# Optimization experiments

Hardware: AMD Instinct MI355X
Metric: run time of the kernel (lower is better)

## Reference

```python
import jax, jax.numpy as jnp
from jax import lax
import numpy as np

K_TOP = 100
NMS_THRESH = 0.5
SUBJECT_CATEGORY_ID = 0


def box_cxcywh_to_xyxy(b):
    cx, cy, w, h = b[..., 0], b[..., 1], b[..., 2], b[..., 3]
    return jnp.stack([cx - 0.5 * w, cy - 0.5 * h, cx + 0.5 * w, cy + 0.5 * h], axis=-1)


def _pairwise_iou(boxes):
    # boxes: [K,4] xyxy; uses the +1 pixel convention from the original numpy NMS
    x1, y1, x2, y2 = boxes[:, 0], boxes[:, 1], boxes[:, 2], boxes[:, 3]
    area = (x2 - x1 + 1.0) * (y2 - y1 + 1.0)
    xx1 = jnp.maximum(x1[:, None], x1[None, :])
    yy1 = jnp.maximum(y1[:, None], y1[None, :])
    xx2 = jnp.minimum(x2[:, None], x2[None, :])
    yy2 = jnp.minimum(y2[:, None], y2[None, :])
    w = jnp.maximum(0.0, xx2 - xx1 + 1.0)
    h = jnp.maximum(0.0, yy2 - yy1 + 1.0)
    inter = w * h
    union = area[:, None] + area[None, :] - inter
    return inter / union


def _nms_keep(sub_boxes, obj_boxes, obj_labels, hoi_scores):
    # Greedy grouped pairwise NMS for one image.
    # Grouping key degenerates to object label (subject cat and verb-row are constant).
    K = sub_boxes.shape[0]
    max_scores = hoi_scores.max(axis=-1)
    order = jnp.argsort(-max_scores)
    ovr = _pairwise_iou(sub_boxes) * _pairwise_iou(obj_boxes)  # [K,K]
    same_group = obj_labels[:, None] == obj_labels[None, :]
    ovr = jnp.where(same_group, ovr, 0.0)
    ovr_s = ovr[order][:, order]
    upper = jnp.triu(jnp.ones((K, K), dtype=bool), k=1)
    sup_mat = (ovr_s > NMS_THRESH) & upper  # suppression only of later (lower-score) items

    def body(i, st):
        suppressed, keep = st
        ki = jnp.logical_not(suppressed[i])
        keep = keep.at[i].set(ki)
        suppressed = suppressed | (ki & sup_mat[i])
        return suppressed, keep

    _, keep_sorted = lax.fori_loop(0, K, body, (jnp.zeros(K, bool), jnp.zeros(K, bool)))
    return jnp.zeros(K, bool).at[order].set(keep_sorted)


def setup_inputs() -> dict:
    key = jax.random.key(0)
    k1, k2, k3, k4, k5, k6 = jax.random.split(key, 6)
    B, Q, C, V = 256, 300, 81, 117
    return {
        "pred_obj_logits": jax.random.normal(k1, (B, Q, C), dtype=jnp.float32),
        "pred_verb_logits": jax.random.normal(k2, (B, Q, V), dtype=jnp.float32),
        "pred_sub_boxes": jax.random.uniform(k3, (B, Q, 4), dtype=jnp.float32),
        "pred_obj_boxes": jax.random.uniform(k4, (B, Q, 4), dtype=jnp.float32),
        "correct_mat": (jax.random.uniform(k5, (V, C), dtype=jnp.float32) > 0.3).astype(jnp.float32),
        "target_sizes": jax.random.randint(k6, (B, 2), 200, 640, dtype=jnp.int32),
    }


def reference(pred_obj_logits, pred_verb_logits, pred_sub_boxes, pred_obj_boxes, correct_mat, target_sizes):
    B, Q, C = pred_obj_logits.shape
    V = pred_verb_logits.shape[-1]

    obj_prob = jax.nn.softmax(pred_obj_logits, axis=-1)       # [B,Q,C]  (no_obj=False)
    verb_scores = jax.nn.sigmoid(pred_verb_logits)            # [B,Q,V]

    topk_values, topk_indexes = lax.top_k(obj_prob.reshape(B, Q * C), K_TOP)  # [B,100]
    topk_boxes = topk_indexes // C
    obj_labels = topk_indexes % C

    vs = jnp.take_along_axis(verb_scores, topk_boxes[..., None], axis=1)      # [B,100,V]
    ob = jnp.take_along_axis(pred_obj_boxes, topk_boxes[..., None], axis=1)   # [B,100,4]
    sb = jnp.take_along_axis(pred_sub_boxes, topk_boxes[..., None], axis=1)

    img_h = target_sizes[:, 0].astype(jnp.float32)
    img_w = target_sizes[:, 1].astype(jnp.float32)
    scale_fct = jnp.stack([img_w, img_h, img_w, img_h], axis=1)  # [B,4]
    sub_boxes = box_cxcywh_to_xyxy(sb) * scale_fct[:, None, :]
    obj_boxes = box_cxcywh_to_xyxy(ob) * scale_fct[:, None, :]

    hoi_scores = vs * topk_values[..., None]                    # [B,100,V]
    # masks[b,k,v] = correct_mat[v, obj_labels[b,k]]
    masks = correct_mat.T[obj_labels]                           # [B,100,V]
    hoi_scores = hoi_scores * masks

    keep = jax.vmap(_nms_keep)(sub_boxes, obj_boxes, obj_labels, hoi_scores)  # [B,100] bool
    final_scores = hoi_scores * keep[..., None].astype(hoi_scores.dtype)

    return final_scores, topk_values, obj_labels, sub_boxes, obj_boxes, keep
```

## Files before the change

kernel.cpp:

```cpp
#include <hip/hip_runtime.h>
#include <cmath>

#pragma clang fp contract(off)

#define NT 1024
constexpr int B_ = 256, Q_ = 300, C_ = 81, V_ = 117, K_ = 100;
constexpr int QC_ = Q_ * C_;
constexpr int KV_ = K_ * V_;
constexpr int CAP = 1024;

using u32 = unsigned int;
using u64 = unsigned long long;
using u16 = unsigned short;
using u8  = unsigned char;

constexpr u32 PCUT_BITS = 0x3C000000u;
constexpr int BIN0 = 480;
constexpr int NB   = 64;

constexpr int OFF_HS   = 0;
constexpr int OFF_HIST = 48600;
constexpr int OFF_RMAX = OFF_HIST + 8192;
constexpr int OFF_RINV = OFF_RMAX + 1200;
constexpr int OFF_BSUB = OFF_RINV + 1208;
constexpr int OFF_BOBJ = OFF_BSUB + 1600;
constexpr int OFF_SUPR = OFF_BOBJ + 1600;
constexpr int OFF_SELV = OFF_SUPR + 1600;
constexpr int OFF_SELI = OFF_SELV + 400;
constexpr int OFF_MAXB = OFF_SELI + 400;
constexpr int OFF_ORD  = OFF_MAXB + 400;
constexpr int OFF_LAB  = OFF_ORD + 104;
constexpr int OFF_MISC = OFF_LAB + 104;
constexpr int SMEM_SZ  = OFF_MISC + 48;
static_assert(SMEM_SZ <= 65536, "LDS overflow");
static_assert((OFF_BSUB & 15) == 0 && (OFF_BOBJ & 15) == 0, "b128 align");

__device__ __forceinline__ u64 shfl_xor_u64(u64 v, int mask) {
    u32 lo = (u32)v, hi = (u32)(v >> 32);
    lo = (u32)__shfl_xor((int)lo, mask, 64);
    hi = (u32)__shfl_xor((int)hi, mask, 64);
    return ((u64)hi << 32) | lo;
}

template <int CTRL>
__device__ __forceinline__ int dpp_i(int x) {
    return __builtin_amdgcn_update_dpp(0, x, CTRL, 0xF, 0xF, true);
}
__device__ __forceinline__ float bfly16(float x){ return __int_as_float(__builtin_amdgcn_ds_swizzle(__float_as_int(x), 0x401F)); }
__device__ __forceinline__ float bfly8 (float x){ return __int_as_float(dpp_i<0x128>(__float_as_int(x))); }
__device__ __forceinline__ float bfly4 (float x){ return __int_as_float(__builtin_amdgcn_ds_swizzle(__float_as_int(x), 0x101F)); }
__device__ __forceinline__ float bfly2 (float x){ return __int_as_float(dpp_i<0x4E>(__float_as_int(x))); }
__device__ __forceinline__ float bfly1 (float x){ return __int_as_float(dpp_i<0xB1>(__float_as_int(x))); }
__device__ __forceinline__ int ibfly4(int x){ return __builtin_amdgcn_ds_swizzle(x, 0x101F); }
__device__ __forceinline__ int ibfly2(int x){ return dpp_i<0x4E>(x); }
__device__ __forceinline__ int ibfly1(int x){ return dpp_i<0xB1>(x); }

__device__ __forceinline__ float iou4(float4 a, float4 b, float areaSum) {
    float xx1 = fmaxf(a.x, b.x);
    float yy1 = fmaxf(a.y, b.y);
    float xx2 = fminf(a.z, b.z);
    float yy2 = fminf(a.w, b.w);
    float w = fmaxf(0.f, xx2 - xx1 + 1.f);
    float h = fmaxf(0.f, yy2 - yy1 + 1.f);
    float inter = w * h;
    return inter / (areaSum - inter);
}

__global__ __launch_bounds__(NT, 4) void hoi_kernel(
    const float* __restrict__ obj_logits,
    const float* __restrict__ verb_logits,
    const float* __restrict__ sub_boxes_in,
    const float* __restrict__ obj_boxes_in,
    const float* __restrict__ cm,
    const int*   __restrict__ tsizes,
    float* __restrict__ out)
{
    const int b = blockIdx.x;
    const int tid = threadIdx.x;

    __shared__ __align__(16) u8 smem[SMEM_SZ];
    float* hs      = (float*)(smem + OFF_HS);
    u32*   hist    = (u32*)(smem + OFF_HIST);
    u64*   cand    = (u64*)(smem + OFF_HIST);
    float* asub    = (float*)(smem + OFF_HIST);
    float* aobj    = (float*)(smem + OFF_HIST + 512);
    float* rowmax  = (float*)(smem + OFF_RMAX);
    float* rinv    = (float*)(smem + OFF_RINV);
    float (*bsub)[4]   = (float(*)[4])(smem + OFF_BSUB);
    float (*bobj)[4]   = (float(*)[4])(smem + OFF_BOBJ);
    u32   (*supcol)[4] = (u32(*)[4])(smem + OFF_SUPR);
    float* sel_val = (float*)(smem + OFF_SELV);
    u32*   sel_idx = (u32*)(smem + OFF_SELI);
    u32*   maxbits = (u32*)(smem + OFF_MAXB);
    u8*    order8  = (u8*)(smem + OFF_ORD);
    u8*    lab8    = (u8*)(smem + OFF_LAB);
    u32*   skeep     = (u32*)(smem + OFF_MISC);
    u32*   keep_bits = (u32*)(smem + OFF_MISC + 16);
    u32*   s_cnt     = (u32*)(smem + OFF_MISC + 32);
    int*   sT        = (int*)(smem + OFF_MISC + 36);
    u64*   wred    = (u64*)(smem + OFF_BOBJ);
    u64*   s_prev  = (u64*)(smem + OFF_SUPR);

    const float* lg = obj_logits + (size_t)b * QC_;

    if (tid < NB) hist[tid] = 0;
    if (tid == 0) *s_cnt = 0;
    __syncthreads();

    const int g = tid >> 5, l = tid & 31;
    const bool have2 = (l < C_ - 64);
    u32 cmask = 0;
    {
        float v0[10], v1[10], v2[10];
        #pragma unroll
        for (int s = 0; s < 10; ++s) {
            int r = g + 32 * s;
            const float* row = lg + (size_t)((r < Q_ ? r : Q_ - 1) * C_);
            v0[s] = row[l];
            v1[s] = row[l + 32];
            v2[s] = have2 ? row[l + 64] : -INFINITY;
        }
        float m[10];
        #pragma unroll
        for (int s = 0; s < 10; ++s) m[s] = fmaxf(fmaxf(v0[s], v1[s]), v2[s]);
        #pragma unroll
        for (int s = 0; s < 10; ++s) m[s] = fmaxf(m[s], bfly16(m[s]));
        #pragma unroll
        for (int s = 0; s < 10; ++s) m[s] = fmaxf(m[s], bfly8(m[s]));
        #pragma unroll
        for (int s = 0; s < 10; ++s) m[s] = fmaxf(m[s], bfly4(m[s]));
        #pragma unroll
        for (int s = 0; s < 10; ++s) m[s] = fmaxf(m[s], bfly2(m[s]));
        #pragma unroll
        for (int s = 0; s < 10; ++s) m[s] = fmaxf(m[s], bfly1(m[s]));
        float e0[10], e1[10], e2[10], sm[10];
        #pragma unroll
        for (int s = 0; s < 10; ++s) {
            e0[s] = expf(v0[s] - m[s]);
            e1[s] = expf(v1[s] - m[s]);
            e2[s] = have2 ? expf(v2[s] - m[s]) : 0.f;
            sm[s] = e0[s] + e1[s] + e2[s];
        }
        #pragma unroll
        for (int s = 0; s < 10; ++s) sm[s] += bfly16(sm[s]);
        #pragma unroll
        for (int s = 0; s < 10; ++s) sm[s] += bfly8(sm[s]);
        #pragma unroll
        for (int s = 0; s < 10; ++s) sm[s] += bfly4(sm[s]);
        #pragma unroll
        for (int s = 0; s < 10; ++s) sm[s] += bfly2(sm[s]);
        #pragma unroll
        for (int s = 0; s < 10; ++s) sm[s] += bfly1(sm[s]);
        #pragma unroll
        for (int s = 0; s < 10; ++s) {
            int r = g + 32 * s;
            if (r < Q_) {
                float ri = 1.f / sm[s];
                float p0 = e0[s] * ri, p1 = e1[s] * ri;
                u32 x0 = __float_as_uint(p0), x1 = __float_as_uint(p1);
                if (x0 >= PCUT_BITS) {
                    atomicAdd(&hist[(x0 >> 21) - BIN0], 1u);
                    cmask |= 1u << (3 * s);
                }
                if (x1 >= PCUT_BITS) {
                    atomicAdd(&hist[(x1 >> 21) - BIN0], 1u);
                    cmask |= 1u << (3 * s + 1);
                }
                if (have2) {
                    float p2 = e2[s] * ri;
                    u32 x2 = __float_as_uint(p2);
                    if (x2 >= PCUT_BITS) {
                        atomicAdd(&hist[(x2 >> 21) - BIN0], 1u);
                        cmask |= 1u << (3 * s + 2);
                    }
                }
                if (l == 0) { rowmax[r] = m[s]; rinv[r] = ri; }
            }
        }
    }
    __syncthreads();

    if (tid < 64) {
        u32 suf = hist[tid];
        #pragma unroll
        for (int off = 1; off < 64; off <<= 1) {
            u32 o = (u32)__shfl_down((int)suf, off, 64);
            suf += (tid + off < 64) ? o : 0;
        }
        u32 nxt = (u32)__shfl_down((int)suf, 1, 64);
        if (tid == 63) nxt = 0;
        if (suf >= (u32)K_ && nxt < (u32)K_) *sT = BIN0 + tid;
    }
    __syncthreads();
    const int T = *sT;

    u32 mk = cmask;
    while (mk) {
        int bpos = (int)__builtin_ctz(mk);
        mk &= mk - 1;
        int s = (bpos * 171) >> 9;
        int c = bpos - 3 * s;
        int r = g + 32 * s;
        int col = l + 32 * c;
        int i = r * C_ + col;
        float p = expf(lg[i] - rowmax[r]) * rinv[r];
        u32 xb = __float_as_uint(p);
        if ((int)(xb >> 21) >= T) {
            u32 pos = atomicAdd(s_cnt, 1u);
            if (pos < (u32)CAP)
                cand[pos] = ((u64)xb << 32) | (u32)(~i);
        }
    }
    __syncthreads();
    const int ncand = (int)*s_cnt;

    auto cswap = [](u64& a, u64& bb, bool up) {
        if ((a > bb) == up) { u64 t = a; a = bb; bb = t; }
    };

    if (ncand <= 256) {
        if (tid < 64) {
            u64 v0 = (tid < ncand) ? cand[tid] : 0ull;
            u64 v1 = (64 + tid < ncand) ? cand[64 + tid] : 0ull;
            u64 v2 = (128 + tid < ncand) ? cand[128 + tid] : 0ull;
            u64 v3 = (192 + tid < ncand) ? cand[192 + tid] : 0ull;
            for (int k = 2; k <= 256; k <<= 1) {
                for (int j = k >> 1; j > 0; j >>= 1) {
                    if (j == 128) {
                        cswap(v0, v2, true);
                        cswap(v1, v3, true);
                    } else if (j == 64) {
                        cswap(v0, v1, true);
                        cswap(v2, v3, (k == 256));
                    } else {
                        auto step = [&](u64& v, int ebase) {
                            u64 pv = shfl_xor_u64(v, j);
                            int e = ebase + tid;
                            bool up = ((e & k) == 0);
                            bool lower = ((e & j) == 0);
                            u64 mn = v < pv ? v : pv;
                            u64 mx = v < pv ? pv : v;
                            v = (lower == up) ? mn : mx;
                        };
                        step(v0, 0); step(v1, 64); step(v2, 128); step(v3, 192);
                    }
                }
            }
            int e2 = 128 + tid;
            if (e2 >= 156) {
                int t = 255 - e2;
                sel_val[t] = __uint_as_float((u32)(v2 >> 32));
                sel_idx[t] = ~(u32)v2;
            }
            int t3 = 255 - (192 + tid);
            sel_val[t3] = __uint_as_float((u32)(v3 >> 32));
            sel_idx[t3] = ~(u32)v3;
        }
    } else if (ncand <= CAP) {
        for (int e = tid; e < CAP; e += NT)
            if (e >= ncand) cand[e] = 0;
        __syncthreads();
        for (int k = 2; k <= CAP; k <<= 1) {
            for (int j = k >> 1; j > 0; j >>= 1) {
                int e = tid, partner = e ^ j;
                if (partner > e) {
                    u64 a = cand[e], bb = cand[partner];
                    bool up = ((e & k) == 0);
                    if ((a > bb) == up) { cand[e] = bb; cand[partner] = a; }
                }
                __syncthreads();
            }
        }
        if (tid < K_) {
            u64 m = cand[CAP - 1 - tid];
            sel_val[tid] = __uint_as_float((u32)(m >> 32));
            sel_idx[tid] = ~(u32)m;
        }
    } else {
        if (tid == 0) *s_prev = ~0ull;
        __syncthreads();
        for (int r = 0; r < K_; r++) {
            u64 prev = *s_prev;
            u64 local = 0;
            for (int i = tid; i < QC_; i += NT) {
                int q = i / C_;
                float p = expf(lg[i] - rowmax[q]) * rinv[q];
                u64 key = ((u64)__float_as_uint(p) << 32) | (u32)(~i);
                if (key < prev && key > local) local = key;
            }
            for (int off = 32; off > 0; off >>= 1) {
                u64 o = shfl_xor_u64(local, off);
                if (o > local) local = o;
            }
            if ((tid & 63) == 0) wred[tid >> 6] = local;
            __syncthreads();
            if (tid == 0) {
                u64 m = wred[0];
                for (int wv = 1; wv < 16; wv++) if (wred[wv] > m) m = wred[wv];
                *s_prev = m;
                u32 idx = ~(u32)m;
                if (idx >= (u32)QC_) idx = 0;
                sel_val[r] = __uint_as_float((u32)(m >> 32));
                sel_idx[r] = idx;
            }
            __syncthreads();
        }
    }
    __syncthreads();

    if (tid < 800) {
        int c = tid >> 3, j = tid & 7;
        u32 idx = sel_idx[c];
        int q = (int)idx / C_, lab = (int)idx - q * C_;
        const float* vrow = verb_logits + ((size_t)b * Q_ + q) * V_;
        float sv = sel_val[c];
        float xv[15], cv[15];
        #pragma unroll
        for (int k = 0; k < 15; ++k) {
            int v = j + 8 * k;
            int vc = v < V_ ? v : V_ - 1;
            xv[k] = vrow[vc];
            cv[k] = cm[vc * C_ + lab];
        }
        float m = 0.f;
        #pragma unroll
        for (int k = 0; k < 15; ++k) {
            int v = j + 8 * k;
            if (v < V_) {
                float hv = (1.f / (1.f + expf(-xv[k]))) * sv * cv[k];
                hs[c * V_ + v] = hv;
                m = fmaxf(m, hv);
            }
        }
        m = fmaxf(m, bfly4(m));
        m = fmaxf(m, bfly2(m));
        m = fmaxf(m, bfly1(m));
        if (j == 0) { maxbits[c] = __float_as_uint(m); lab8[c] = (u8)lab; }
    } else if (tid < 900) {
        int t = tid - 800;
        int idx = (int)sel_idx[t];
        int q = idx / C_;
        float iw = (float)tsizes[b * 2 + 1];
        float ih = (float)tsizes[b * 2 + 0];
        float4 sb = ((const float4*)sub_boxes_in)[(size_t)b * Q_ + q];
        float x1 = (sb.x - 0.5f * sb.z) * iw, y1 = (sb.y - 0.5f * sb.w) * ih;
        float x2 = (sb.x + 0.5f * sb.z) * iw, y2 = (sb.y + 0.5f * sb.w) * ih;
        bsub[t][0] = x1; bsub[t][1] = y1; bsub[t][2] = x2; bsub[t][3] = y2;
        asub[t] = (x2 - x1 + 1.f) * (y2 - y1 + 1.f);
        supcol[t][0] = 0; supcol[t][1] = 0; supcol[t][2] = 0; supcol[t][3] = 0;
    } else if (tid < 1000) {
        int t = tid - 900;
        int idx = (int)sel_idx[t];
        int q = idx / C_;
        float iw = (float)tsizes[b * 2 + 1];
        float ih = (float)tsizes[b * 2 + 0];
        float4 ob = ((const float4*)obj_boxes_in)[(size_t)b * Q_ + q];
        float x1 = (ob.x - 0.5f * ob.z) * iw, y1 = (ob.y - 0.5f * ob.w) * ih;
        float x2 = (ob.x + 0.5f * ob.z) * iw, y2 = (ob.y + 0.5f * ob.w) * ih;
        bobj[t][0] = x1; bobj[t][1] = y1; bobj[t][2] = x2; bobj[t][3] = y2;
        aobj[t] = (x2 - x1 + 1.f) * (y2 - y1 + 1.f);
    } else if (tid < 1004) {
        keep_bits[tid - 1000] = 0;
    }
    __syncthreads();

    if (tid < 800) {
        int r = tid >> 3, j = tid & 7;
        u64 kr = ((u64)maxbits[r] << 32) | (u32)(~r);
        int rank = 0;
        for (int k = 0; k < 13; k++) {
            int jj = j * 13 + k;
            if (jj < K_) {
                u64 kj = ((u64)maxbits[jj] << 32) | (u32)(~jj);
                rank += (kj > kr) ? 1 : 0;
            }
        }
        rank += ibfly4(rank);
        rank += ibfly2(rank);
        rank += ibfly1(rank);
        if (j == 0) order8[rank] = (u8)r;
    }
    __syncthreads();

    float* o0 = out;
    float* o1 = out + (size_t)B_ * KV_;
    float* o2 = o1 + (size_t)B_ * K_;
    float* o3 = o2 + (size_t)B_ * K_;
    float* o4 = o3 + (size_t)B_ * K_ * 4;
    float* o5 = o4 + (size_t)B_ * K_ * 4;

    if (tid < K_) {
        o1[(size_t)b * K_ + tid] = sel_val[tid];
        o2[(size_t)b * K_ + tid] = (float)(sel_idx[tid] % (u32)C_);
    }
    if (tid >= 128 && tid < 128 + K_ * 4) {
        int t = tid - 128;
        int r = t >> 2, k = t & 3;
        o3[((size_t)b * K_) * 4 + t] = bsub[r][k];
        o4[((size_t)b * K_) * 4 + t] = bobj[r][k];
    }

    for (int e = tid; e < K_ * K_; e += NT) {
        int i = e / K_, j = e - i * K_;
        if (j > i) {
            int ri = order8[i], rj = order8[j];
            u32 li = lab8[ri], lj = lab8[rj];
            if (li == lj) {
                float4 s_i = *(const float4*)bsub[ri];
                float4 s_j = *(const float4*)bsub[rj];
                float4 b_i = *(const float4*)bobj[ri];
                float4 b_j = *(const float4*)bobj[rj];
                float o = iou4(s_i, s_j, asub[ri] + asub[rj]) *
                          iou4(b_i, b_j, aobj[ri] + aobj[rj]);
                if (o > 0.5f)
                    atomicOr(&supcol[j][i >> 5], 1u << (i & 31));
            }
        }
    }
    __syncthreads();

    if (tid < 64) {
        u32 cA[4], cB[4];
        #pragma unroll
        for (int w = 0; w < 4; ++w) cA[w] = supcol[tid][w];
        #pragma unroll
        for (int w = 0; w < 4; ++w) cB[w] = (tid < K_ - 64) ? supcol[tid + 64][w] : 0u;
        bool sA = false, sB = false;
        u32 km[4] = {0, 0, 0, 0};
        #pragma unroll
        for (int i = 0; i < 64; ++i) {
            u64 bal = __ballot(sA);
            if (!((bal >> i) & 1)) {
                km[i >> 5] |= 1u << (i & 31);
                sA = sA || ((cA[i >> 5] >> (i & 31)) & 1u);
                sB = sB || ((cB[i >> 5] >> (i & 31)) & 1u);
            }
        }
        #pragma unroll
        for (int i = 64; i < K_; ++i) {
            u64 bal = __ballot(sB);
            if (!((bal >> (i - 64)) & 1)) {
                km[i >> 5] |= 1u << (i & 31);
                sA = sA || ((cA[i >> 5] >> (i & 31)) & 1u);
                sB = sB || ((cB[i >> 5] >> (i & 31)) & 1u);
            }
        }
        if (tid == 0) { skeep[0] = km[0]; skeep[1] = km[1]; skeep[2] = km[2]; skeep[3] = km[3]; }
    }
    __syncthreads();
    if (tid < K_) {
        if ((skeep[tid >> 5] >> (tid & 31)) & 1u) {
            int r = order8[tid];
            atomicOr(&keep_bits[r >> 5], 1u << (r & 31));
        }
    }
    __syncthreads();

    constexpr int KV4_ = KV_ / 4;
    for (int f4 = tid; f4 < KV4_; f4 += NT) {
        int base = f4 * 4;
        float4 h = *(const float4*)(hs + base);
        int r0 = base / V_, m0 = base - r0 * V_;
        int r1 = r0 + ((m0 + 1) >= V_ ? 1 : 0);
        int r2 = r0 + ((m0 + 2) >= V_ ? 1 : 0);
        int r3 = r0 + ((m0 + 3) >= V_ ? 1 : 0);
        float4 o;
        o.x = ((keep_bits[r0 >> 5] >> (r0 & 31)) & 1u) ? h.x : 0.f;
        o.y = ((keep_bits[r1 >> 5] >> (r1 & 31)) & 1u) ? h.y : 0.f;
        o.z = ((keep_bits[r2 >> 5] >> (r2 & 31)) & 1u) ? h.z : 0.f;
        o.w = ((keep_bits[r3 >> 5] >> (r3 & 31)) & 1u) ? h.w : 0.f;
        *(float4*)(o0 + (size_t)b * KV_ + base) = o;
    }
    if (tid < K_) {
        bool kp = (keep_bits[tid >> 5] >> (tid & 31)) & 1u;
        o5[(size_t)b * K_ + tid] = kp ? 1.f : 0.f;
    }
}

extern "C" void kernel_launch(void* const* d_in, const int* in_sizes, int n_in,
                              void* d_out, int out_size, void* d_ws, size_t ws_size,
                              hipStream_t stream) {
    const float* obj_logits  = (const float*)d_in[0];
    const float* verb_logits = (const float*)d_in[1];
    const float* sub_boxes   = (const float*)d_in[2];
    const float* obj_boxes   = (const float*)d_in[3];
    const float* cm          = (const float*)d_in[4];
    const int*   ts          = (const int*)d_in[5];
    hipLaunchKernelGGL(hoi_kernel, dim3(B_), dim3(NT), 0, stream,
                       obj_logits, verb_logits, sub_boxes, obj_boxes, cm, ts,
                       (float*)d_out);
}
```

Measured before the change: 137.9 us.

## Replace bitonic candidate sort with parallel rank selection and pad row arrays

Replaces the two bitonic-sort paths for top-k candidates with a rank-by-counting scheme. Each candidate thread counts how many keys exceed its own and writes itself to that rank slot if it falls within the top K. This removes the many barrier-separated sort stages, at the cost of O(n^2) LDS reads per candidate set. It also pads the rowmax/rinv indexing (r + r/32) to reduce LDS bank conflicts and shifts the LDS offsets to match.

After: 129.6 us. -6.0%, faster.

```diff
diff --git a/kernel.cpp b/kernel.cpp
--- a/kernel.cpp
+++ b/kernel.cpp
@@ -19,10 +19,10 @@
 constexpr int NB   = 64;
 
 constexpr int OFF_HS   = 0;
-constexpr int OFF_HIST = 48600;
+constexpr int OFF_HIST = 46816;
 constexpr int OFF_RMAX = OFF_HIST + 8192;
-constexpr int OFF_RINV = OFF_RMAX + 1200;
-constexpr int OFF_BSUB = OFF_RINV + 1208;
+constexpr int OFF_RINV = OFF_RMAX + 1240;
+constexpr int OFF_BSUB = OFF_RINV + 1240;
 constexpr int OFF_BOBJ = OFF_BSUB + 1600;
 constexpr int OFF_SUPR = OFF_BOBJ + 1600;
 constexpr int OFF_SELV = OFF_SUPR + 1600;
@@ -34,6 +34,9 @@
 constexpr int SMEM_SZ  = OFF_MISC + 48;
 static_assert(SMEM_SZ <= 65536, "LDS overflow");
 static_assert((OFF_BSUB & 15) == 0 && (OFF_BOBJ & 15) == 0, "b128 align");
+static_assert(OFF_HIST >= 46800, "cand/hs overlap");
+
+__device__ __forceinline__ int RM(int r) { return r + (r >> 5); }
 
 __device__ __forceinline__ u64 shfl_xor_u64(u64 v, int mask) {
     u32 lo = (u32)v, hi = (u32)(v >> 32);
@@ -174,7 +177,7 @@
                         cmask |= 1u << (3 * s + 2);
                     }
                 }
-                if (l == 0) { rowmax[r] = m[s]; rinv[r] = ri; }
+                if (l == 0) { rowmax[RM(r)] = m[s]; rinv[RM(r)] = ri; }
             }
         }
     }
@@ -203,7 +206,7 @@
         int r = g + 32 * s;
         int col = l + 32 * c;
         int i = r * C_ + col;
-        float p = expf(lg[i] - rowmax[r]) * rinv[r];
+        float p = expf(lg[i] - rowmax[RM(r)]) * rinv[RM(r)];
         u32 xb = __float_as_uint(p);
         if ((int)(xb >> 21) >= T) {
             u32 pos = atomicAdd(s_cnt, 1u);
@@ -214,67 +217,24 @@
     __syncthreads();
     const int ncand = (int)*s_cnt;
 
-    auto cswap = [](u64& a, u64& bb, bool up) {
-        if ((a > bb) == up) { u64 t = a; a = bb; bb = t; }
-    };
-
-    if (ncand <= 256) {
-        if (tid < 64) {
-            u64 v0 = (tid < ncand) ? cand[tid] : 0ull;
-            u64 v1 = (64 + tid < ncand) ? cand[64 + tid] : 0ull;
-            u64 v2 = (128 + tid < ncand) ? cand[128 + tid] : 0ull;
-            u64 v3 = (192 + tid < ncand) ? cand[192 + tid] : 0ull;
-            for (int k = 2; k <= 256; k <<= 1) {
-                for (int j = k >> 1; j > 0; j >>= 1) {
-                    if (j == 128) {
-                        cswap(v0, v2, true);
-                        cswap(v1, v3, true);
-                    } else if (j == 64) {
-                        cswap(v0, v1, true);
-                        cswap(v2, v3, (k == 256));
-                    } else {
-                        auto step = [&](u64& v, int ebase) {
-                            u64 pv = shfl_xor_u64(v, j);
-                            int e = ebase + tid;
-                            bool up = ((e & k) == 0);
-                            bool lower = ((e & j) == 0);
-                            u64 mn = v < pv ? v : pv;
-                            u64 mx = v < pv ? pv : v;
-                            v = (lower == up) ? mn : mx;
-                        };
-                        step(v0, 0); step(v1, 64); step(v2, 128); step(v3, 192);
-                    }
-                }
-            }
-            int e2 = 128 + tid;
-            if (e2 >= 156) {
-                int t = 255 - e2;
-                sel_val[t] = __uint_as_float((u32)(v2 >> 32));
-                sel_idx[t] = ~(u32)v2;
-            }
-            int t3 = 255 - (192 + tid);
-            sel_val[t3] = __uint_as_float((u32)(v3 >> 32));
-            sel_idx[t3] = ~(u32)v3;
-        }
-    } else if (ncand <= CAP) {
-        for (int e = tid; e < CAP; e += NT)
-            if (e >= ncand) cand[e] = 0;
-        __syncthreads();
-        for (int k = 2; k <= CAP; k <<= 1) {
-            for (int j = k >> 1; j > 0; j >>= 1) {
-                int e = tid, partner = e ^ j;
-                if (partner > e) {
-                    u64 a = cand[e], bb = cand[partner];
-                    bool up = ((e & k) == 0);
-                    if ((a > bb) == up) { cand[e] = bb; cand[partner] = a; }
-                }
-                __syncthreads();
-            }
-        }
-        if (tid < K_) {
-            u64 m = cand[CAP - 1 - tid];
-            sel_val[tid] = __uint_as_float((u32)(m >> 32));
-            sel_idx[tid] = ~(u32)m;
+    if (ncand <= CAP) {
+        if (tid < ncand) {
+            u64 mykey = cand[tid];
+            int rank = 0;
+            int f = 0;
+            for (; f + 4 <= ncand; f += 4) {
+                u64 k0 = cand[f], k1 = cand[f + 1];
+                u64 k2 = cand[f + 2], k3 = cand[f + 3];
+                rank += (k0 > mykey) ? 1 : 0;
+                rank += (k1 > mykey) ? 1 : 0;
+                rank += (k2 > mykey) ? 1 : 0;
+                rank += (k3 > mykey) ? 1 : 0;
+            }
+            for (; f < ncand; ++f) rank += (cand[f] > mykey) ? 1 : 0;
+            if (rank < K_) {
+                sel_val[rank] = __uint_as_float((u32)(mykey >> 32));
+                sel_idx[rank] = ~(u32)mykey;
+            }
         }
     } else {
         if (tid == 0) *s_prev = ~0ull;
@@ -284,7 +244,7 @@
             u64 local = 0;
             for (int i = tid; i < QC_; i += NT) {
                 int q = i / C_;
-                float p = expf(lg[i] - rowmax[q]) * rinv[q];
+                float p = expf(lg[i] - rowmax[RM(q)]) * rinv[RM(q)];
                 u64 key = ((u64)__float_as_uint(p) << 32) | (u32)(~i);
                 if (key < prev && key > local) local = key;
             }
```
